# Kernel tuning notes

Hardware: AMD Instinct MI355X
Metric: run time of the kernel (lower is better)

Reference implementation:

```python
import jax, jax.numpy as jnp
import numpy as np

DIM = 2048
N_HEADS = 16
N_KV = 4
HEAD_DIM = DIM // N_HEADS  # 128
G = N_HEADS // N_KV        # queries per kv head
EPS = 1e-6
ROPE_BASE = 10000.0


def _rms_norm(x, w):
    # x: [..., head_dim]
    norm = jax.lax.rsqrt(jnp.mean(x * x, axis=-1, keepdims=True) + EPS)
    return x * norm * w


def _rope_tables(seq_len, dtype):
    inv_freq = 1.0 / (ROPE_BASE ** (jnp.arange(0, HEAD_DIM, 2, dtype=jnp.float32) / HEAD_DIM))
    t = jnp.arange(seq_len, dtype=jnp.float32)
    freqs = jnp.einsum('i,j->ij', t, inv_freq)          # [S, hd/2]
    emb = jnp.concatenate([freqs, freqs], axis=-1)       # [S, hd]
    return jnp.cos(emb).astype(dtype), jnp.sin(emb).astype(dtype)


def _rotate_half(x):
    x1, x2 = x[..., : HEAD_DIM // 2], x[..., HEAD_DIM // 2:]
    return jnp.concatenate([-x2, x1], axis=-1)


def setup_inputs() -> dict:
    key = jax.random.key(0)
    ks = jax.random.split(key, 7)
    x = jax.random.normal(ks[0], (2, 2048, DIM), dtype=jnp.float32)
    s = 0.02
    Wq = jax.random.normal(ks[1], (DIM, DIM), dtype=jnp.float32) * s
    Wk = jax.random.normal(ks[2], (DIM, N_KV * HEAD_DIM), dtype=jnp.float32) * s
    Wv = jax.random.normal(ks[3], (DIM, N_KV * HEAD_DIM), dtype=jnp.float32) * s
    Wo = jax.random.normal(ks[4], (DIM, DIM), dtype=jnp.float32) * s
    q_norm_w = jnp.ones((HEAD_DIM,), dtype=jnp.float32)
    k_norm_w = jnp.ones((HEAD_DIM,), dtype=jnp.float32)
    return {"x": x, "Wq": Wq, "Wk": Wk, "Wv": Wv, "Wo": Wo,
            "q_norm_w": q_norm_w, "k_norm_w": k_norm_w}


def reference(x, Wq, Wk, Wv, Wo, q_norm_w, k_norm_w):
    B, S, _ = x.shape
    q = (x @ Wq).reshape(B, S, N_HEADS, HEAD_DIM)
    k = (x @ Wk).reshape(B, S, N_KV, HEAD_DIM)
    v = (x @ Wv).reshape(B, S, N_KV, HEAD_DIM)

    q = _rms_norm(q, q_norm_w)
    k = _rms_norm(k, k_norm_w)

    q = q.transpose(0, 2, 1, 3)  # [B, H, S, hd]
    k = k.transpose(0, 2, 1, 3)  # [B, KV, S, hd]
    v = v.transpose(0, 2, 1, 3)

    cos, sin = _rope_tables(S, x.dtype)  # [S, hd], broadcasts over B,H
    q = q * cos + _rotate_half(q) * sin
    k = k * cos + _rotate_half(k) * sin

    # GQA: group queries by kv head instead of repeating K/V (same math as repeat_interleave)
    qg = q.reshape(B, N_KV, G, S, HEAD_DIM)
    scale = HEAD_DIM ** -0.5
    scores = jnp.einsum('bkgqd,bkkd2->bkgqk2'.replace('k2', 'K').replace('d2', 'd'),
                        qg, k) if False else jnp.einsum('bkgqd,bkKd->bkgqK', qg, k) * scale
    attn = jax.nn.softmax(scores, axis=-1)               # [B, KV, G, S, S]
    out = jnp.einsum('bkgqK,bkKd->bkgqd', attn, v)       # [B, KV, G, S, hd]
    out = out.reshape(B, N_HEADS, S, HEAD_DIM).transpose(0, 2, 1, 3).reshape(B, S, DIM)
    return out @ Wo
```

## Files before the change

kernel.cpp:

```cpp
#include <hip/hip_runtime.h>
#include <stdint.h>

#define LOG2E 1.4426950408889634f

typedef __attribute__((ext_vector_type(8))) short short8;
typedef __attribute__((ext_vector_type(4))) float floatx4;
typedef unsigned int u32;

__device__ __forceinline__ float bf2f(unsigned short h) {
  union { unsigned int u; float f; } v; v.u = ((unsigned int)h) << 16; return v.f;
}
__device__ __forceinline__ unsigned short f2bf(float f) {
  union { float f; unsigned int u; } v; v.f = f;
  unsigned int r = v.u + 0x7FFFu + ((v.u >> 16) & 1u);
  return (unsigned short)(r >> 16);
}
__device__ __forceinline__ u32 fbits(float f) {
  union { float f; u32 u; } v; v.f = f; return v.u;
}
__device__ __forceinline__ void async16(void* lds, const void* g) {
  __builtin_amdgcn_global_load_lds((const __attribute__((address_space(1))) u32*)g,
                                   (__attribute__((address_space(3))) u32*)lds, 16, 0, 0);
}

__global__ __launch_bounds__(256) void cvt_f32_bf16(const float* __restrict__ src,
                                                    unsigned short* __restrict__ dst, int n) {
  int i = (blockIdx.x * 256 + threadIdx.x) * 8;
  if (i >= n) return;
  float4 a = ((const float4*)(src + i))[0];
  float4 b = ((const float4*)(src + i))[1];
  union { uint4 v; unsigned short u[8]; } o;
  o.u[0] = f2bf(a.x); o.u[1] = f2bf(a.y); o.u[2] = f2bf(a.z); o.u[3] = f2bf(a.w);
  o.u[4] = f2bf(b.x); o.u[5] = f2bf(b.y); o.u[6] = f2bf(b.z); o.u[7] = f2bf(b.w);
  *(uint4*)(dst + i) = o.v;
}

__global__ __launch_bounds__(256) void transpose_cvt4(const float* __restrict__ Wq,
                                                      const float* __restrict__ Wk,
                                                      const float* __restrict__ Wv,
                                                      const float* __restrict__ Wo,
                                                      unsigned short* __restrict__ WTqkv,
                                                      unsigned short* __restrict__ WoT) {
  const int R = 2048;
  int bid = blockIdx.x;
  const float* src; unsigned short* dst; int C;
  if (bid < 1024) { src = Wq; dst = WTqkv; C = 2048; }
  else if (bid < 1280) { src = Wk; dst = WTqkv + (size_t)2048 * 2048; C = 512; bid -= 1024; }
  else if (bid < 1536) { src = Wv; dst = WTqkv + (size_t)2048 * 2048 + (size_t)512 * 2048; C = 512; bid -= 1280; }
  else { src = Wo; dst = WoT; C = 2048; bid -= 1536; }

  __shared__ unsigned short tile[64][65];
  int tc = C >> 6;
  int br = bid / tc, bc = bid % tc;
  int r0 = br << 6, c0 = bc << 6;
  int i = threadIdx.x >> 2, cc = (threadIdx.x & 3) << 4;
  const float4* g = (const float4*)(src + (size_t)(r0 + i) * C + c0 + cc);
  float4 f0 = g[0], f1 = g[1], f2 = g[2], f3 = g[3];
  unsigned short u[16];
  u[0]=f2bf(f0.x); u[1]=f2bf(f0.y); u[2]=f2bf(f0.z); u[3]=f2bf(f0.w);
  u[4]=f2bf(f1.x); u[5]=f2bf(f1.y); u[6]=f2bf(f1.z); u[7]=f2bf(f1.w);
  u[8]=f2bf(f2.x); u[9]=f2bf(f2.y); u[10]=f2bf(f2.z); u[11]=f2bf(f2.w);
  u[12]=f2bf(f3.x); u[13]=f2bf(f3.y); u[14]=f2bf(f3.z); u[15]=f2bf(f3.w);
#pragma unroll
  for (int j = 0; j < 16; ++j) tile[i][cc + j] = u[j];
  __syncthreads();
  union { uint4 v[2]; unsigned short u[16]; } buf;
#pragma unroll
  for (int j = 0; j < 16; ++j) buf.u[j] = tile[cc + j][i];
  uint4* o = (uint4*)(dst + (size_t)(c0 + i) * R + r0 + cc);
  o[0] = buf.v[0]; o[1] = buf.v[1];
}

template <typename OutT>
__global__ __launch_bounds__(256) void gemm_nt(const unsigned short* __restrict__ A,
                                               const unsigned short* __restrict__ BT,
                                               OutT* __restrict__ C,
                                               int M, int N, int K) {
  __shared__ unsigned short As[2][128 * 32];
  __shared__ unsigned short Bs[2][128 * 32];
  const int nb = N >> 7;
  const int bm = blockIdx.x / nb, bn = blockIdx.x % nb;
  const int m0 = bm << 7, n0 = bn << 7;
  const int tid = threadIdx.x;
  const int lane = tid & 63, wave = tid >> 6;
  const int l15 = lane & 15, quad = lane >> 4;
  const int wm = (wave >> 1) << 6, wn = (wave & 1) << 6;

  floatx4 acc[4][4];
#pragma unroll
  for (int i = 0; i < 4; ++i)
#pragma unroll
    for (int j = 0; j < 4; ++j) acc[i][j] = (floatx4){0.f, 0.f, 0.f, 0.f};

  const int Lc0 = wave * 128 + lane;
#pragma unroll
  for (int i = 0; i < 2; ++i) {
    int Lc = Lc0 + i * 64;
    int row = Lc >> 2;
    int c = (lane & 3) ^ ((row >> 1) & 3);
    async16(As[0] + (size_t)Lc * 8, A + (size_t)(m0 + row) * K + c * 8);
    async16(Bs[0] + (size_t)Lc * 8, BT + (size_t)(n0 + row) * K + c * 8);
  }

  const int nk = K >> 5;
  for (int it = 0; it < nk; ++it) {
    const int cur = it & 1;
    __syncthreads();
    if (it + 1 < nk) {
      int k1 = (it + 1) << 5;
#pragma unroll
      for (int i = 0; i < 2; ++i) {
        int Lc = Lc0 + i * 64;
        int row = Lc >> 2;
        int c = (lane & 3) ^ ((row >> 1) & 3);
        async16(As[cur ^ 1] + (size_t)Lc * 8, A + (size_t)(m0 + row) * K + k1 + c * 8);
        async16(Bs[cur ^ 1] + (size_t)Lc * 8, BT + (size_t)(n0 + row) * K + k1 + c * 8);
      }
    }
    short8 af[4], bf[4];
#pragma unroll
    for (int mt = 0; mt < 4; ++mt) {
      int m = wm + mt * 16 + l15;
      af[mt] = *(const short8*)(&As[cur][(m * 4 + (quad ^ ((m >> 1) & 3))) * 8]);
    }
#pragma unroll
    for (int nt = 0; nt < 4; ++nt) {
      int n = wn + nt * 16 + l15;
      bf[nt] = *(const short8*)(&Bs[cur][(n * 4 + (quad ^ ((n >> 1) & 3))) * 8]);
    }
#pragma unroll
    for (int mt = 0; mt < 4; ++mt)
#pragma unroll
      for (int nt = 0; nt < 4; ++nt)
        acc[mt][nt] = __builtin_amdgcn_mfma_f32_16x16x32_bf16(af[mt], bf[nt], acc[mt][nt], 0, 0, 0);
  }
#pragma unroll
  for (int mt = 0; mt < 4; ++mt)
#pragma unroll
    for (int nt = 0; nt < 4; ++nt)
#pragma unroll
      for (int r = 0; r < 4; ++r) {
        int m = m0 + wm + mt * 16 + quad * 4 + r;
        int n = n0 + wn + nt * 16 + l15;
        float v = acc[mt][nt][r];
        if constexpr (sizeof(OutT) == 2)
          C[(size_t)m * N + n] = (OutT)f2bf(v);
        else
          C[(size_t)m * N + n] = (OutT)v;
      }
}

template <typename OutT>
__global__ __launch_bounds__(512, 2) void gemm_nt_256(const unsigned short* __restrict__ A,
                                                      const unsigned short* __restrict__ BT,
                                                      OutT* __restrict__ C,
                                                      int M, int N, int K) {
  (void)M;
  __shared__ unsigned short As[2][16384];
  __shared__ unsigned short Bs[2][16384];
  const int nbn = N >> 8;
  const int nwg = gridDim.x;
  int wg = blockIdx.x;
  {
    int cpx = nwg >> 3;
    wg = (wg & 7) * cpx + (wg >> 3);
  }
  const int m0 = (wg / nbn) << 8;
  const int n0 = (wg % nbn) << 8;
  const int tid = threadIdx.x;
  const int lane = tid & 63, wave = tid >> 6;
  const int l15 = lane & 15, quad = lane >> 4;
  const int wr = wave >> 2, wc = wave & 3;
  const int rA = wr * 128 + l15;
  const int rB = wc * 64 + l15;

  floatx4 acc[8][4];
#pragma unroll
  for (int i = 0; i < 8; ++i)
#pragma unroll
    for (int j = 0; j < 4; ++j) acc[i][j] = (floatx4){0.f, 0.f, 0.f, 0.f};

  const unsigned short* Ag = A + (size_t)m0 * K;
  const unsigned short* Bg = BT + (size_t)n0 * K;

  auto STAGE = [&](unsigned short* dst, const unsigned short* g) {
#pragma unroll
    for (int j = 0; j < 2; ++j) {
      int idx = j * 512 + tid;
      int r = idx >> 2;
      int c = (idx & 3) ^ (r & 3);
      async16(dst + (size_t)idx * 8, g + (size_t)r * K + c * 8);
    }
  };
  auto RD = [&](const unsigned short* buf, int row, int ch) -> short8 {
    int kh = ch >> 2;
    int cq = (ch & 3) ^ (row & 3);
    return *(const short8*)(buf + kh * 8192 + row * 32 + cq * 8);
  };

#define BAR() __builtin_amdgcn_s_barrier()
#define LGKM0() do { asm volatile("s_waitcnt lgkmcnt(0)" ::: "memory"); \
                     __builtin_amdgcn_sched_barrier(0); } while (0)

  STAGE(As[0], Ag);
  STAGE(Bs[0], Bg);
  STAGE(As[0] + 8192, Ag + 32);
  STAGE(Bs[0] + 8192, Bg + 32);
  STAGE(As[1], Ag + 64);
  STAGE(Bs[1], Bg + 64);
  STAGE(As[1] + 8192, Ag + 96);
  asm volatile("s_waitcnt vmcnt(6)" ::: "memory");
  BAR();

  short8 af[8], bfr[4];
  const int NT = K >> 6;
  for (int t = 0; t < NT; ++t) {
    unsigned short* Ac = As[t & 1];
    unsigned short* Bc = Bs[t & 1];
    unsigned short* Bn = Bs[(t & 1) ^ 1];
    const unsigned short* Agt = Ag + (size_t)(t + 2) * 64;
    const unsigned short* Bgt = Bg + (size_t)(t + 2) * 64;

#pragma unroll
    for (int mf = 0; mf < 8; ++mf) af[mf] = RD(Ac, rA + mf * 16, quad);
#pragma unroll
    for (int nf = 0; nf < 4; ++nf) bfr[nf] = RD(Bc, rB + nf * 16, quad);
    if (t + 1 < NT) STAGE(Bn + 8192, Bg + (size_t)(t + 1) * 64 + 32);
    BAR(); LGKM0();
    __builtin_amdgcn_s_setprio(1);
#pragma unroll
    for (int mf = 0; mf < 4; ++mf)
#pragma unroll
      for (int nf = 0; nf < 4; ++nf)
        acc[mf][nf] = __builtin_amdgcn_mfma_f32_16x16x32_bf16(af[mf], bfr[nf], acc[mf][nf], 0, 0, 0);
    __builtin_amdgcn_s_setprio(0);
    BAR();

    if (t + 2 < NT) STAGE(Ac, Agt);
    BAR(); LGKM0();
    __builtin_amdgcn_s_setprio(1);
#pragma unroll
    for (int mf = 4; mf < 8; ++mf)
#pragma unroll
      for (int nf = 0; nf < 4; ++nf)
        acc[mf][nf] = __builtin_amdgcn_mfma_f32_16x16x32_bf16(af[mf], bfr[nf], acc[mf][nf], 0, 0, 0);
    __builtin_amdgcn_s_setprio(0);
    BAR();

#pragma unroll
    for (int mf = 0; mf < 8; ++mf) af[mf] = RD(Ac, rA + mf * 16, 4 + quad);
#pragma unroll
    for (int nf = 0; nf < 4; ++nf) bfr[nf] = RD(Bc, rB + nf * 16, 4 + quad);
    if (t + 2 < NT) STAGE(Bc, Bgt);
    BAR(); LGKM0();
    __builtin_amdgcn_s_setprio(1);
#pragma unroll
    for (int mf = 0; mf < 4; ++mf)
#pragma unroll
      for (int nf = 0; nf < 4; ++nf)
        acc[mf][nf] = __builtin_amdgcn_mfma_f32_16x16x32_bf16(af[mf], bfr[nf], acc[mf][nf], 0, 0, 0);
    __builtin_amdgcn_s_setprio(0);
    BAR();

    if (t + 2 < NT) STAGE(Ac + 8192, Agt + 32);
    if (t + 2 < NT) {
      asm volatile("s_waitcnt vmcnt(6)" ::: "memory");
    } else if (t + 1 < NT) {
      asm volatile("s_waitcnt vmcnt(0)" ::: "memory");
    }
    BAR(); LGKM0();
    __builtin_amdgcn_s_setprio(1);
#pragma unroll
    for (int mf = 4; mf < 8; ++mf)
#pragma unroll
      for (int nf = 0; nf < 4; ++nf)
        acc[mf][nf] = __builtin_amdgcn_mfma_f32_16x16x32_bf16(af[mf], bfr[nf], acc[mf][nf], 0, 0, 0);
    __builtin_amdgcn_s_setprio(0);
    BAR();
  }
#undef BAR
#undef LGKM0

#pragma unroll
  for (int mf = 0; mf < 8; ++mf)
#pragma unroll
    for (int nf = 0; nf < 4; ++nf)
#pragma unroll
      for (int r = 0; r < 4; ++r) {
        int m = m0 + wr * 128 + mf * 16 + quad * 4 + r;
        int n = n0 + wc * 64 + nf * 16 + l15;
        float v = acc[mf][nf][r];
        if constexpr (sizeof(OutT) == 2)
          C[(size_t)m * N + n] = (OutT)f2bf(v);
        else
          C[(size_t)m * N + n] = (OutT)v;
      }
}

__global__ __launch_bounds__(256) void norm_rope(const unsigned short* __restrict__ qkv,
                                                 const float* __restrict__ qw,
                                                 const float* __restrict__ kw,
                                                 unsigned short* __restrict__ qT,
                                                 unsigned short* __restrict__ kT) {
  const int S = 2048;
  int wid = blockIdx.x * 4 + (threadIdx.x >> 6);
  int lane = threadIdx.x & 63;
  int slot = wid % 20;
  int bs = wid / 20;
  int s = bs & (S - 1), b = bs >> 11;
  const unsigned short* src;
  unsigned short* dst;
  const float* w;
  float scale;
  if (slot < 16) {
    src = qkv + (size_t)bs * 3072 + slot * 128;
    dst = qT + ((size_t)(b * 16 + slot) * S + s) * 128;
    w = qw; scale = 0.08838834764831845f * 1.4426950408889634f;
  } else {
    int kvi = slot - 16;
    src = qkv + (size_t)bs * 3072 + 2048 + kvi * 128;
    dst = kT + ((size_t)(b * 4 + kvi) * S + s) * 128;
    w = kw; scale = 1.0f;
  }
  float x1 = bf2f(src[lane]), x2 = bf2f(src[lane + 64]);
  float ss = x1 * x1 + x2 * x2;
#pragma unroll
  for (int m = 1; m < 64; m <<= 1) ss += __shfl_xor(ss, m, 64);
  float rms = rsqrtf(ss * (1.0f / 128.0f) + 1e-6f);
  float y1 = x1 * rms * w[lane];
  float y2 = x2 * rms * w[lane + 64];
  float ang = (float)s * exp2f((float)lane * -0.2076205059304601f);
  float c = cosf(ang), sn = sinf(ang);
  float o1 = (y1 * c - y2 * sn) * scale;
  float o2 = (y2 * c + y1 * sn) * scale;
  dst[lane] = f2bf(o1);
  dst[lane + 64] = f2bf(o2);
}

__global__ __launch_bounds__(256) void v_transpose(const unsigned short* __restrict__ qkv,
                                                   unsigned short* __restrict__ vT) {
  const int S = 2048;
  int bid = blockIdx.x;
  int dt = bid & 1, st = (bid >> 1) & 31, kv = (bid >> 6) & 3, b = bid >> 8;
  int s0 = st << 6, d0 = dt << 6;
  __shared__ unsigned short tile[64][65];
  int i = threadIdx.x >> 2, cc = (threadIdx.x & 3) << 4;
  union { uint4 v[2]; unsigned short u[16]; } buf;
  const uint4* g = (const uint4*)(qkv + ((size_t)(b * S) + s0 + i) * 3072 + 2560 + kv * 128 + d0 + cc);
  buf.v[0] = g[0]; buf.v[1] = g[1];
#pragma unroll
  for (int j = 0; j < 16; ++j) tile[i][cc + j] = buf.u[j];
  __syncthreads();
#pragma unroll
  for (int j = 0; j < 16; ++j) buf.u[j] = tile[cc + j][i];
  uint4* o = (uint4*)(vT + ((size_t)(b * 4 + kv) * 128 + d0 + i) * S + s0 + cc);
  o[0] = buf.v[0]; o[1] = buf.v[1];
}

__global__ __launch_bounds__(256, 2) void flash_attn(const unsigned short* __restrict__ qT,
                                                     const unsigned short* __restrict__ kT,
                                                     const unsigned short* __restrict__ vT,
                                                     unsigned short* __restrict__ ao) {
  const int S = 2048;
  int bid = blockIdx.x;
  int qt = bid & 15, h = (bid >> 4) & 15, b = bid >> 8;
  int kv = h >> 2;
  int tid = threadIdx.x;
  int lane = tid & 63, wave = tid >> 6;
  int l15 = lane & 15, quad = lane >> 4;

  __shared__ unsigned short Ks[2][64 * 128];
  __shared__ unsigned short VTs[2][128 * 64];
  __shared__ unsigned short Ps[4][32 * 64];
  unsigned short* Psw = Ps[wave];

  short8 bq[2][4];
  const unsigned short* qbase = qT + ((size_t)(b * 16 + h) * S + qt * 128 + wave * 32) * 128;
#pragma unroll
  for (int nt = 0; nt < 2; ++nt)
#pragma unroll
    for (int kk = 0; kk < 4; ++kk)
      bq[nt][kk] = *(const short8*)(qbase + (size_t)(nt * 16 + l15) * 128 + kk * 32 + quad * 8);

  floatx4 O[2][8];
#pragma unroll
  for (int mt = 0; mt < 2; ++mt)
#pragma unroll
    for (int dt = 0; dt < 8; ++dt) O[mt][dt] = (floatx4){0.f, 0.f, 0.f, 0.f};
  float l_acc[2] = {0.f, 0.f};

  const size_t kbase = (size_t)(b * 4 + kv) * S * 128;
  const size_t vbase = (size_t)(b * 4 + kv) * 128 * S;

#pragma unroll
  for (int i = 0; i < 4; ++i) {
    int Lc = (wave * 4 + i) * 64 + lane;
    int row = Lc >> 4, cjk = (lane & 15) ^ (row & 7);
    async16(Ks[0] + (size_t)Lc * 8, kT + kbase + (size_t)row * 128 + cjk * 8);
    int d = Lc >> 3, cjv = (lane & 7) ^ (d & 7);
    async16(VTs[0] + (size_t)Lc * 8, vT + vbase + (size_t)d * S + cjv * 8);
  }

  for (int kt = 0; kt < 32; ++kt) {
    int cur = kt & 1;
    __syncthreads();
    if (kt + 1 < 32) {
#pragma unroll
      for (int i = 0; i < 4; ++i) {
        int Lc = (wave * 4 + i) * 64 + lane;
        int row = Lc >> 4, cjk = (lane & 15) ^ (row & 7);
        async16(Ks[cur ^ 1] + (size_t)Lc * 8,
                kT + kbase + (size_t)((kt + 1) * 64 + row) * 128 + cjk * 8);
        int d = Lc >> 3, cjv = (lane & 7) ^ (d & 7);
        async16(VTs[cur ^ 1] + (size_t)Lc * 8,
                vT + vbase + (size_t)d * S + (kt + 1) * 64 + cjv * 8);
      }
    }

    floatx4 st[4][2];
#pragma unroll
    for (int a = 0; a < 4; ++a)
#pragma unroll
      for (int nt = 0; nt < 2; ++nt) st[a][nt] = (floatx4){0.f, 0.f, 0.f, 0.f};
    __builtin_amdgcn_s_setprio(1);
#pragma unroll
    for (int kk = 0; kk < 4; ++kk)
#pragma unroll
      for (int a = 0; a < 4; ++a) {
        int m = a * 16 + l15;
        short8 ak = *(const short8*)(&Ks[cur][(m * 16 + ((kk * 4 + quad) ^ (m & 7))) * 8]);
#pragma unroll
        for (int nt = 0; nt < 2; ++nt)
          st[a][nt] = __builtin_amdgcn_mfma_f32_16x16x32_bf16(ak, bq[nt][kk], st[a][nt], 0, 0, 0);
      }
    __builtin_amdgcn_s_setprio(0);

#pragma unroll
    for (int nt = 0; nt < 2; ++nt) {
      int m = nt * 16 + l15;
#pragma unroll
      for (int a = 0; a < 4; ++a) {
        float e0 = __builtin_amdgcn_exp2f(st[a][nt][0]);
        float e1 = __builtin_amdgcn_exp2f(st[a][nt][1]);
        float e2 = __builtin_amdgcn_exp2f(st[a][nt][2]);
        float e3 = __builtin_amdgcn_exp2f(st[a][nt][3]);
        l_acc[nt] += (e0 + e1) + (e2 + e3);
        u32 p01 = __builtin_amdgcn_perm(fbits(e1) + 0x8000u, fbits(e0) + 0x8000u, 0x07060302u);
        u32 p23 = __builtin_amdgcn_perm(fbits(e3) + 0x8000u, fbits(e2) + 0x8000u, 0x07060302u);
        int c = (a * 2 + (quad >> 1)) ^ (m & 7);
        uint2 pk; pk.x = p01; pk.y = p23;
        *(uint2*)(&Psw[(m * 8 + c) * 8 + (quad & 1) * 4]) = pk;
      }
    }

    __builtin_amdgcn_s_setprio(1);
#pragma unroll
    for (int kk2 = 0; kk2 < 2; ++kk2) {
      short8 ap[2];
#pragma unroll
      for (int mt = 0; mt < 2; ++mt) {
        int m = mt * 16 + l15;
        ap[mt] = *(const short8*)(&Psw[(m * 8 + ((kk2 * 4 + quad) ^ (m & 7))) * 8]);
      }
#pragma unroll
      for (int dt = 0; dt < 8; ++dt) {
        int n = dt * 16 + l15;
        short8 bv = *(const short8*)(&VTs[cur][(n * 8 + ((kk2 * 4 + quad) ^ (n & 7))) * 8]);
#pragma unroll
        for (int mt = 0; mt < 2; ++mt)
          O[mt][dt] = __builtin_amdgcn_mfma_f32_16x16x32_bf16(ap[mt], bv, O[mt][dt], 0, 0, 0);
      }
    }
    __builtin_amdgcn_s_setprio(0);
  }

  float linv[2];
#pragma unroll
  for (int nt = 0; nt < 2; ++nt) {
    float l = l_acc[nt];
    l += __shfl_xor(l, 16, 64);
    l += __shfl_xor(l, 32, 64);
    linv[nt] = 1.f / l;
  }
#pragma unroll
  for (int mt = 0; mt < 2; ++mt)
#pragma unroll
    for (int r = 0; r < 4; ++r) {
      float inv = __shfl(linv[mt], quad * 4 + r, 64);
      int s = qt * 128 + wave * 32 + mt * 16 + quad * 4 + r;
#pragma unroll
      for (int dt = 0; dt < 8; ++dt) {
        int d = dt * 16 + l15;
        ao[((size_t)(b * S + s) * 16 + h) * 128 + d] = f2bf(O[mt][dt][r] * inv);
      }
    }
}

extern "C" void kernel_launch(void* const* d_in, const int* in_sizes, int n_in,
                              void* d_out, int out_size, void* d_ws, size_t ws_size,
                              hipStream_t stream) {
  const float* x  = (const float*)d_in[0];
  const float* Wq = (const float*)d_in[1];
  const float* Wk = (const float*)d_in[2];
  const float* Wv = (const float*)d_in[3];
  const float* Wo = (const float*)d_in[4];
  const float* qw = (const float*)d_in[5];
  const float* kw = (const float*)d_in[6];
  float* out = (float*)d_out;

  unsigned short* p = (unsigned short*)d_ws;
  unsigned short* xbf   = p; p += (size_t)4096 * 2048;
  unsigned short* WTqkv = p; p += (size_t)3072 * 2048;
  unsigned short* WoT   = p; p += (size_t)2048 * 2048;
  unsigned short* qkv   = p; p += (size_t)4096 * 3072;
  unsigned short* qTb   = p; p += (size_t)2 * 16 * 2048 * 128;
  unsigned short* kTb   = p; p += (size_t)2 * 4 * 2048 * 128;
  unsigned short* vTb   = p; p += (size_t)2 * 4 * 2048 * 128;
  unsigned short* ao    = p; p += (size_t)4096 * 2048;

  cvt_f32_bf16<<<4096, 256, 0, stream>>>(x, xbf, 4096 * 2048);
  transpose_cvt4<<<2560, 256, 0, stream>>>(Wq, Wk, Wv, Wo, WTqkv, WoT);

  gemm_nt_256<unsigned short><<<192, 512, 0, stream>>>(xbf, WTqkv, qkv, 4096, 3072, 2048);

  norm_rope<<<20480, 256, 0, stream>>>(qkv, qw, kw, qTb, kTb);
  v_transpose<<<512, 256, 0, stream>>>(qkv, vTb);

  flash_attn<<<512, 256, 0, stream>>>(qTb, kTb, vTb, ao);

  gemm_nt<float><<<512, 256, 0, stream>>>(ao, WoT, out, 4096, 2048, 2048);
}
```

Baseline: 329.1 us.

## Restructure 256x256 GEMM main loop into quadrant-ordered MFMA phases with 8-way swizzle

Changes the LDS tile layout from two 32-wide K halves with a 4-way XOR swizzle to a single 64-wide row layout with an 8-way XOR swizzle. The main loop now loads A/B fragments per quadrant (top/bottom M half, left/right N half), covering the full K=64 in each phase, and orders the four MFMA phases so that fragments are reused across adjacent phases. Global prefetch staging is split into row halves interleaved between phases, and the waitcnt thresholds and barriers are adjusted to match. The aim is fewer LDS reads per MFMA, fewer LDS bank conflicts and better overlap of loads with compute. The cost is more registers held live and delicate vmcnt/lgkmcnt accounting that must match the new staging order.

```diff
diff --git a/kernel.cpp b/kernel.cpp
--- a/kernel.cpp
+++ b/kernel.cpp
@@ -156,8 +156,8 @@
                                                       OutT* __restrict__ C,
                                                       int M, int N, int K) {
   (void)M;
-  __shared__ unsigned short As[2][16384];
-  __shared__ unsigned short Bs[2][16384];
+  __shared__ unsigned short As[2][256 * 64];
+  __shared__ unsigned short Bs[2][256 * 64];
   const int nbn = N >> 8;
   const int nwg = gridDim.x;
   int wg = blockIdx.x;
@@ -183,103 +183,113 @@
   const unsigned short* Ag = A + (size_t)m0 * K;
   const unsigned short* Bg = BT + (size_t)n0 * K;
 
-  auto STAGE = [&](unsigned short* dst, const unsigned short* g) {
+  auto STAGE = [&](unsigned short* dst, const unsigned short* g, int h) {
 #pragma unroll
     for (int j = 0; j < 2; ++j) {
       int idx = j * 512 + tid;
-      int r = idx >> 2;
-      int c = (idx & 3) ^ (r & 3);
-      async16(dst + (size_t)idx * 8, g + (size_t)r * K + c * 8);
+      int row = h * 128 + (idx >> 3);
+      int cl = (idx & 7) ^ (row & 7);
+      async16(dst + (size_t)h * 8192 + (size_t)idx * 8, g + (size_t)row * K + cl * 8);
     }
   };
-  auto RD = [&](const unsigned short* buf, int row, int ch) -> short8 {
-    int kh = ch >> 2;
-    int cq = (ch & 3) ^ (row & 3);
-    return *(const short8*)(buf + kh * 8192 + row * 32 + cq * 8);
+  auto RD = [&](const unsigned short* buf, int row, int ks) -> short8 {
+    int sc = ((ks << 2) + quad) ^ (row & 7);
+    return *(const short8*)(buf + row * 64 + sc * 8);
   };
 
 #define BAR() __builtin_amdgcn_s_barrier()
-#define LGKM0() do { asm volatile("s_waitcnt lgkmcnt(0)" ::: "memory"); \
-                     __builtin_amdgcn_sched_barrier(0); } while (0)
-
-  STAGE(As[0], Ag);
-  STAGE(Bs[0], Bg);
-  STAGE(As[0] + 8192, Ag + 32);
-  STAGE(Bs[0] + 8192, Bg + 32);
-  STAGE(As[1], Ag + 64);
-  STAGE(Bs[1], Bg + 64);
-  STAGE(As[1] + 8192, Ag + 96);
-  asm volatile("s_waitcnt vmcnt(6)" ::: "memory");
+#define WAITL0() asm volatile("s_waitcnt lgkmcnt(0)" ::: "memory")
+
+  STAGE(As[0], Ag, 0); STAGE(As[0], Ag, 1);
+  STAGE(Bs[0], Bg, 0); STAGE(Bs[0], Bg, 1);
+  STAGE(As[1], Ag + 64, 0); STAGE(As[1], Ag + 64, 1);
+  asm volatile("s_waitcnt vmcnt(4)" ::: "memory");
   BAR();
 
-  short8 af[8], bfr[4];
   const int NT = K >> 6;
+  short8 a0[4][2], a1[4][2], b0[2][2], b1[2][2];
   for (int t = 0; t < NT; ++t) {
-    unsigned short* Ac = As[t & 1];
-    unsigned short* Bc = Bs[t & 1];
-    unsigned short* Bn = Bs[(t & 1) ^ 1];
-    const unsigned short* Agt = Ag + (size_t)(t + 2) * 64;
-    const unsigned short* Bgt = Bg + (size_t)(t + 2) * 64;
-
-#pragma unroll
-    for (int mf = 0; mf < 8; ++mf) af[mf] = RD(Ac, rA + mf * 16, quad);
-#pragma unroll
-    for (int nf = 0; nf < 4; ++nf) bfr[nf] = RD(Bc, rB + nf * 16, quad);
-    if (t + 1 < NT) STAGE(Bn + 8192, Bg + (size_t)(t + 1) * 64 + 32);
-    BAR(); LGKM0();
+    const unsigned short* Ac = As[t & 1];
+    const unsigned short* Bc = Bs[t & 1];
+    unsigned short* Ast = As[t & 1];
+    unsigned short* Bst = Bs[(t + 1) & 1];
+
+#pragma unroll
+    for (int mf = 0; mf < 4; ++mf)
+#pragma unroll
+      for (int ks = 0; ks < 2; ++ks) a0[mf][ks] = RD(Ac, rA + mf * 16, ks);
+#pragma unroll
+    for (int nf = 0; nf < 2; ++nf)
+#pragma unroll
+      for (int ks = 0; ks < 2; ++ks) b0[nf][ks] = RD(Bc, rB + nf * 16, ks);
+    if (t + 1 < NT) STAGE(Bst, Bg + (size_t)(t + 1) * 64, 0);
+    asm volatile("s_waitcnt lgkmcnt(8)" ::: "memory");
+    BAR(); WAITL0();
     __builtin_amdgcn_s_setprio(1);
 #pragma unroll
     for (int mf = 0; mf < 4; ++mf)
 #pragma unroll
-      for (int nf = 0; nf < 4; ++nf)
-        acc[mf][nf] = __builtin_amdgcn_mfma_f32_16x16x32_bf16(af[mf], bfr[nf], acc[mf][nf], 0, 0, 0);
+      for (int nf = 0; nf < 2; ++nf)
+#pragma unroll
+        for (int ks = 0; ks < 2; ++ks)
+          acc[mf][nf] = __builtin_amdgcn_mfma_f32_16x16x32_bf16(a0[mf][ks], b0[nf][ks], acc[mf][nf], 0, 0, 0);
     __builtin_amdgcn_s_setprio(0);
     BAR();
 
-    if (t + 2 < NT) STAGE(Ac, Agt);
-    BAR(); LGKM0();
+#pragma unroll
+    for (int mf = 0; mf < 4; ++mf)
+#pragma unroll
+      for (int ks = 0; ks < 2; ++ks) a1[mf][ks] = RD(Ac, rA + 64 + mf * 16, ks);
+    if (t + 1 < NT) STAGE(Bst, Bg + (size_t)(t + 1) * 64, 1);
+    BAR(); WAITL0();
     __builtin_amdgcn_s_setprio(1);
 #pragma unroll
-    for (int mf = 4; mf < 8; ++mf)
-#pragma unroll
-      for (int nf = 0; nf < 4; ++nf)
-        acc[mf][nf] = __builtin_amdgcn_mfma_f32_16x16x32_bf16(af[mf], bfr[nf], acc[mf][nf], 0, 0, 0);
+    for (int mf = 0; mf < 4; ++mf)
+#pragma unroll
+      for (int nf = 0; nf < 2; ++nf)
+#pragma unroll
+        for (int ks = 0; ks < 2; ++ks)
+          acc[4 + mf][nf] = __builtin_amdgcn_mfma_f32_16x16x32_bf16(a1[mf][ks], b0[nf][ks], acc[4 + mf][nf], 0, 0, 0);
     __builtin_amdgcn_s_setprio(0);
     BAR();
 
 #pragma unroll
-    for (int mf = 0; mf < 8; ++mf) af[mf] = RD(Ac, rA + mf * 16, 4 + quad);
-#pragma unroll
-    for (int nf = 0; nf < 4; ++nf) bfr[nf] = RD(Bc, rB + nf * 16, 4 + quad);
-    if (t + 2 < NT) STAGE(Bc, Bgt);
-    BAR(); LGKM0();
+    for (int nf = 0; nf < 2; ++nf)
+#pragma unroll
+      for (int ks = 0; ks < 2; ++ks) b1[nf][ks] = RD(Bc, rB + 32 + nf * 16, ks);
+    if (t + 2 < NT) STAGE(Ast, Ag + (size_t)(t + 2) * 64, 0);
+    BAR(); WAITL0();
     __builtin_amdgcn_s_setprio(1);
 #pragma unroll
     for (int mf = 0; mf < 4; ++mf)
 #pragma unroll
-      for (int nf = 0; nf < 4; ++nf)
-        acc[mf][nf] = __builtin_amdgcn_mfma_f32_16x16x32_bf16(af[mf], bfr[nf], acc[mf][nf], 0, 0, 0);
+      for (int nf = 0; nf < 2; ++nf)
+#pragma unroll
+        for (int ks = 0; ks < 2; ++ks)
+          acc[4 + mf][2 + nf] = __builtin_amdgcn_mfma_f32_16x16x32_bf16(a1[mf][ks], b1[nf][ks], acc[4 + mf][2 + nf], 0, 0, 0);
     __builtin_amdgcn_s_setprio(0);
     BAR();
 
-    if (t + 2 < NT) STAGE(Ac + 8192, Agt + 32);
     if (t + 2 < NT) {
-      asm volatile("s_waitcnt vmcnt(6)" ::: "memory");
-    } else if (t + 1 < NT) {
+      STAGE(Ast, Ag + (size_t)(t + 2) * 64, 1);
+      asm volatile("s_waitcnt vmcnt(4)" ::: "memory");
+    } else {
       asm volatile("s_waitcnt vmcnt(0)" ::: "memory");
     }
-    BAR(); LGKM0();
+    BAR();
     __builtin_amdgcn_s_setprio(1);
 #pragma unroll
-    for (int mf = 4; mf < 8; ++mf)
-#pragma unroll
-      for (int nf = 0; nf < 4; ++nf)
-        acc[mf][nf] = __builtin_amdgcn_mfma_f32_16x16x32_bf16(af[mf], bfr[nf], acc[mf][nf], 0, 0, 0);
+    for (int mf = 0; mf < 4; ++mf)
+#pragma unroll
+      for (int nf = 0; nf < 2; ++nf)
+#pragma unroll
+        for (int ks = 0; ks < 2; ++ks)
+          acc[mf][2 + nf] = __builtin_amdgcn_mfma_f32_16x16x32_bf16(a0[mf][ks], b1[nf][ks], acc[mf][2 + nf], 0, 0, 0);
     __builtin_amdgcn_s_setprio(0);
     BAR();
   }
 #undef BAR
-#undef LGKM0
+#undef WAITL0
 
 #pragma unroll
   for (int mf = 0; mf < 8; ++mf)
```

Result: faster. 320.8 us (-2.5%).
